# Kernel tuning notes

Measured on AMD Instinct MI355X. Metric: run time of the kernel, lower is better.

Reference implementation:

```python
import jax, jax.numpy as jnp
import numpy as np

N = 8192          # num nodes
F_IN = 512        # num_features
H = 256           # hidden_dim
D = 64            # embedding_dim
E = 262144        # num edges (avg degree 32)


def setup_inputs() -> dict:
    key = jax.random.key(0)
    ks = jax.random.split(key, 6)
    x = jax.random.normal(ks[0], (N, F_IN), dtype=jnp.float32)
    adj_rows = jax.random.randint(ks[1], (E,), 0, N)
    adj_cols = jax.random.randint(ks[2], (E,), 0, N)
    adj_vals = jax.random.uniform(ks[3], (E,), dtype=jnp.float32)
    W1 = jax.random.normal(ks[4], (F_IN, H), dtype=jnp.float32) / np.sqrt(F_IN)
    b1 = jnp.zeros((H,), dtype=jnp.float32)
    W2 = jax.random.normal(ks[5], (H, D), dtype=jnp.float32) / np.sqrt(H)
    b2 = jnp.zeros((D,), dtype=jnp.float32)
    return {"x": x, "adj_rows": adj_rows, "adj_cols": adj_cols,
            "adj_vals": adj_vals, "W1": W1, "b1": b1, "W2": W2, "b2": b2}


def _spmm(rows, cols, vals, dense):
    # sparse [N,N] @ dense [N,F] via gather + segment-sum (COO spmm)
    gathered = vals[:, None] * dense[cols]           # [E, F]
    return jax.ops.segment_sum(gathered, rows, num_segments=N)


def reference(x, adj_rows, adj_cols, adj_vals, W1, b1, W2, b2):
    # GCN layer 1: linear -> spmm -> relu (dropout is identity in eval mode)
    h = _spmm(adj_rows, adj_cols, adj_vals, x @ W1 + b1)   # [N, H]
    h = jax.nn.relu(h)
    # GCN layer 2: linear -> spmm
    z = _spmm(adj_rows, adj_cols, adj_vals, h @ W2 + b2)   # [N, D]
    # decode: sigmoid(z z^T)
    adj_rec = jax.nn.sigmoid(z @ z.T)                       # [N, N]
    return (z, adj_rec)
```

## Files before the change

### kernel.cpp

```cpp
#include <hip/hip_runtime.h>
#include <hip/hip_bf16.h>

#define NN 8192
#define FIN 512
#define HD 256
#define DD 64
#define NE 262144
#define BCAP 128

typedef __bf16 bf16_t;
typedef __bf16 bf16x8 __attribute__((ext_vector_type(8)));
typedef __bf16 bf16x4 __attribute__((ext_vector_type(4)));
typedef float f32x4 __attribute__((ext_vector_type(4)));

__global__ __launch_bounds__(256) void prep_kernel(const float* __restrict__ x, bf16_t* __restrict__ x_b,
                                                   const float* __restrict__ W1, bf16_t* __restrict__ w1t,
                                                   const float* __restrict__ W2, bf16_t* __restrict__ w2t,
                                                   int* __restrict__ deg) {
    int b = blockIdx.x;
    if (b < 2048) {
        int i = (b * 256 + threadIdx.x) * 8;
        float4 v0 = *reinterpret_cast<const float4*>(x + i);
        float4 v1 = *reinterpret_cast<const float4*>(x + i + 4);
        bf16x8 o = {(bf16_t)v0.x, (bf16_t)v0.y, (bf16_t)v0.z, (bf16_t)v0.w,
                    (bf16_t)v1.x, (bf16_t)v1.y, (bf16_t)v1.z, (bf16_t)v1.w};
        *reinterpret_cast<bf16x8*>(x_b + i) = o;
    } else if (b < 2048 + 128) {
        int o4 = ((b - 2048) * 256 + threadIdx.x) * 4;
        int r = o4 & 511;
        int c = o4 >> 9;
        bf16x4 o = {(bf16_t)W1[(r + 0) * HD + c], (bf16_t)W1[(r + 1) * HD + c],
                    (bf16_t)W1[(r + 2) * HD + c], (bf16_t)W1[(r + 3) * HD + c]};
        *reinterpret_cast<bf16x4*>(w1t + o4) = o;
    } else if (b < 2048 + 128 + 16) {
        int o4 = ((b - 2048 - 128) * 256 + threadIdx.x) * 4;
        int r = o4 & 255;
        int c = o4 >> 8;
        bf16x4 o = {(bf16_t)W2[(r + 0) * DD + c], (bf16_t)W2[(r + 1) * DD + c],
                    (bf16_t)W2[(r + 2) * DD + c], (bf16_t)W2[(r + 3) * DD + c]};
        *reinterpret_cast<bf16x4*>(w2t + o4) = o;
    } else {
        int o = ((b - 2048 - 128 - 16) * 256 + threadIdx.x) * 4;
        *reinterpret_cast<int4*>(deg + o) = {0, 0, 0, 0};
    }
}

__global__ __launch_bounds__(256) void gemm1_scatter(const bf16_t* __restrict__ A,
                                                     const bf16_t* __restrict__ Bt,
                                                     const float* __restrict__ bias,
                                                     bf16_t* __restrict__ C,
                                                     const int* __restrict__ rows, const int* __restrict__ cols,
                                                     const float* __restrict__ vals,
                                                     int* __restrict__ deg, int* __restrict__ scol,
                                                     float* __restrict__ sval) {
    int b = blockIdx.x;
    if (b >= 512) {
        int e = (b - 512) * 256 + threadIdx.x;
        int r = rows[e];
        int p = atomicAdd(&deg[r], 1);
        scol[r * BCAP + p] = cols[e];
        sval[r * BCAP + p] = vals[e];
        return;
    }
    const int K = FIN, N = HD;
    int wave = threadIdx.x >> 6;
    int lane = threadIdx.x & 63;
    int lr = lane & 15;
    int lq = lane >> 4;
    int m0 = (b & 127) * 64 + wave * 16;
    int n0 = (b >> 7) * 64;

    f32x4 acc[4];
#pragma unroll
    for (int t = 0; t < 4; t++) acc[t] = {0.f, 0.f, 0.f, 0.f};

    const bf16_t* Abase = A + (size_t)(m0 + lr) * K + lq * 8;
    const bf16_t* Bbase = Bt + (size_t)(n0 + lr) * K + lq * 8;
    for (int k0 = 0; k0 < K; k0 += 32) {
        bf16x8 a = *reinterpret_cast<const bf16x8*>(Abase + k0);
#pragma unroll
        for (int t = 0; t < 4; t++) {
            bf16x8 bb = *reinterpret_cast<const bf16x8*>(Bbase + (size_t)t * 16 * K + k0);
            acc[t] = __builtin_amdgcn_mfma_f32_16x16x32_bf16(a, bb, acc[t], 0, 0, 0);
        }
    }
#pragma unroll
    for (int t = 0; t < 4; t++) {
        int col = n0 + t * 16 + lr;
        float bv = bias[col];
#pragma unroll
        for (int r = 0; r < 4; r++) {
            int row = m0 + lq * 4 + r;
            C[(size_t)row * N + col] = (bf16_t)(acc[t][r] + bv);
        }
    }
}


__global__ __launch_bounds__(256) void spmm_h_kernel(const int* __restrict__ deg,
                                                     const int* __restrict__ scol,
                                                     const float* __restrict__ sval,
                                                     const bf16_t* __restrict__ h0,
                                                     bf16_t* __restrict__ h) {
    int r = blockIdx.x;
    int wv = threadIdx.x >> 6;
    int lane = threadIdx.x & 63;
    int nd = deg[r];
    int base = r * BCAP;
    float a0 = 0.f, a1 = 0.f, a2 = 0.f, a3 = 0.f;
#pragma unroll 2
    for (int e = wv; e < nd; e += 4) {
        int c = scol[base + e];
        float v = sval[base + e];
        bf16x4 hv = *reinterpret_cast<const bf16x4*>(h0 + (size_t)c * HD + lane * 4);
        a0 += v * (float)hv[0];
        a1 += v * (float)hv[1];
        a2 += v * (float)hv[2];
        a3 += v * (float)hv[3];
    }
    __shared__ float red[4][256];
    red[wv][lane * 4 + 0] = a0;
    red[wv][lane * 4 + 1] = a1;
    red[wv][lane * 4 + 2] = a2;
    red[wv][lane * 4 + 3] = a3;
    __syncthreads();
    if (wv == 0) {
        int f = lane * 4;
        bf16x4 o = {(bf16_t)fmaxf(red[0][f + 0] + red[1][f + 0] + red[2][f + 0] + red[3][f + 0], 0.f),
                    (bf16_t)fmaxf(red[0][f + 1] + red[1][f + 1] + red[2][f + 1] + red[3][f + 1], 0.f),
                    (bf16_t)fmaxf(red[0][f + 2] + red[1][f + 2] + red[2][f + 2] + red[3][f + 2], 0.f),
                    (bf16_t)fmaxf(red[0][f + 3] + red[1][f + 3] + red[2][f + 3] + red[3][f + 3], 0.f)};
        *reinterpret_cast<bf16x4*>(h + (size_t)r * HD + f) = o;
    }
}

__global__ __launch_bounds__(256) void spmm_z_kernel(const int* __restrict__ deg,
                                                     const int* __restrict__ scol,
                                                     const float* __restrict__ sval,
                                                     const bf16_t* __restrict__ z0,
                                                     float* __restrict__ z_out,
                                                     bf16_t* __restrict__ z_b) {
    int wv = threadIdx.x >> 6;
    int lane = threadIdx.x & 63;
    int lq = lane >> 4;
    int lr = lane & 15;
    int r = blockIdx.x * 16 + wv * 4 + lq;
    int nd = deg[r];
    int base = r * BCAP;
    float a0 = 0.f, a1 = 0.f, a2 = 0.f, a3 = 0.f;
    for (int e = 0; e < nd; e++) {
        int c = scol[base + e];
        float v = sval[base + e];
        bf16x4 zv = *reinterpret_cast<const bf16x4*>(z0 + (size_t)c * DD + lr * 4);
        a0 += v * (float)zv[0];
        a1 += v * (float)zv[1];
        a2 += v * (float)zv[2];
        a3 += v * (float)zv[3];
    }
    f32x4 of = {a0, a1, a2, a3};
    *reinterpret_cast<f32x4*>(z_out + (size_t)r * DD + lr * 4) = of;
    bf16x4 ob = {(bf16_t)a0, (bf16_t)a1, (bf16_t)a2, (bf16_t)a3};
    *reinterpret_cast<bf16x4*>(z_b + (size_t)r * DD + lr * 4) = ob;
}

template <int ACT, typename OutT, int MW>
__global__ __launch_bounds__(256) void gemm_bt(const bf16_t* __restrict__ A,
                                               const bf16_t* __restrict__ Bt,
                                               const float* __restrict__ bias,
                                               OutT* __restrict__ C,
                                               int M, int N, int K) {
    int wave = threadIdx.x >> 6;
    int lane = threadIdx.x & 63;
    int lr = lane & 15;
    int lq = lane >> 4;
    int m0 = blockIdx.x * (64 * MW) + wave * (16 * MW);
    int n0 = blockIdx.y * 64;

    f32x4 acc[MW][4];
#pragma unroll
    for (int i = 0; i < MW; i++)
#pragma unroll
        for (int t = 0; t < 4; t++) acc[i][t] = {0.f, 0.f, 0.f, 0.f};

    const bf16_t* Abase = A + (size_t)(m0 + lr) * K + lq * 8;
    const bf16_t* Bbase = Bt + (size_t)(n0 + lr) * K + lq * 8;

    for (int k0 = 0; k0 < K; k0 += 32) {
        bf16x8 a[MW];
#pragma unroll
        for (int i = 0; i < MW; i++)
            a[i] = *reinterpret_cast<const bf16x8*>(Abase + (size_t)i * 16 * K + k0);
#pragma unroll
        for (int t = 0; t < 4; t++) {
            bf16x8 b = *reinterpret_cast<const bf16x8*>(Bbase + (size_t)t * 16 * K + k0);
#pragma unroll
            for (int i = 0; i < MW; i++)
                acc[i][t] = __builtin_amdgcn_mfma_f32_16x16x32_bf16(a[i], b, acc[i][t], 0, 0, 0);
        }
    }

    if (ACT == 2) {
        __shared__ float ldsT[256 / 64 * 16 * MW][65];
        int rbase = wave * 16 * MW;
#pragma unroll
        for (int i = 0; i < MW; i++)
#pragma unroll
            for (int t = 0; t < 4; t++)
#pragma unroll
                for (int r = 0; r < 4; r++) {
                    float v = acc[i][t][r];
                    v = 1.f / (1.f + __expf(-v));
                    ldsT[rbase + i * 16 + lq * 4 + r][t * 16 + lr] = v;
                }
        int c4 = (lane & 15) * 4;
        int rr = lane >> 4;
#pragma unroll
        for (int j = 0; j < 4 * MW; j++) {
            int row_l = rbase + j * 4 + rr;
            f32x4 v = *reinterpret_cast<const f32x4*>(&ldsT[row_l][c4]);
            size_t gaddr = (size_t)(blockIdx.x * (64 * MW) + row_l) * N + n0 + c4;
            *reinterpret_cast<f32x4*>(&C[gaddr]) = v;
        }
    } else {
#pragma unroll
        for (int i = 0; i < MW; i++) {
#pragma unroll
            for (int t = 0; t < 4; t++) {
                int col = n0 + t * 16 + lr;
                float bv = bias ? bias[col] : 0.f;
#pragma unroll
                for (int r = 0; r < 4; r++) {
                    int row = m0 + i * 16 + lq * 4 + r;
                    C[(size_t)row * N + col] = (OutT)(acc[i][t][r] + bv);
                }
            }
        }
    }
}


extern "C" void kernel_launch(void* const* d_in, const int* in_sizes, int n_in,
                              void* d_out, int out_size, void* d_ws, size_t ws_size,
                              hipStream_t stream) {
    const float* x   = (const float*)d_in[0];
    const int* rows  = (const int*)d_in[1];
    const int* cols  = (const int*)d_in[2];
    const float* vals = (const float*)d_in[3];
    const float* W1  = (const float*)d_in[4];
    const float* b1  = (const float*)d_in[5];
    const float* W2  = (const float*)d_in[6];
    const float* b2  = (const float*)d_in[7];

    float* out_z   = (float*)d_out;
    float* out_adj = out_z + (size_t)NN * DD;

    char* ws = (char*)d_ws;
    size_t off = 0;
    auto alloc = [&](size_t bytes) { void* p = ws + off; off += (bytes + 255) & ~(size_t)255; return p; };
    bf16_t* x_b   = (bf16_t*)alloc((size_t)NN * FIN * 2);
    bf16_t* w1t   = (bf16_t*)alloc((size_t)HD * FIN * 2);
    bf16_t* w2t   = (bf16_t*)alloc((size_t)DD * HD * 2);
    bf16_t* h0    = (bf16_t*)alloc((size_t)NN * HD * 2);
    bf16_t* h_b   = (bf16_t*)alloc((size_t)NN * HD * 2);
    bf16_t* z0    = (bf16_t*)alloc((size_t)NN * DD * 2);
    bf16_t* z_b   = (bf16_t*)alloc((size_t)NN * DD * 2);
    int* deg      = (int*)alloc((size_t)NN * 4);
    int* scol     = (int*)alloc((size_t)NN * BCAP * 4);
    float* sval   = (float*)alloc((size_t)NN * BCAP * 4);

    prep_kernel<<<2048 + 128 + 16 + 8, 256, 0, stream>>>(x, x_b, W1, w1t, W2, w2t, deg);

    gemm1_scatter<<<512 + 1024, 256, 0, stream>>>(x_b, w1t, b1, h0,
                                                  rows, cols, vals, deg, scol, sval);

    spmm_h_kernel<<<NN, 256, 0, stream>>>(deg, scol, sval, h0, h_b);

    gemm_bt<0, bf16_t, 1><<<dim3(NN / 64, DD / 64), 256, 0, stream>>>(h_b, w2t, b2, z0, NN, DD, HD);

    spmm_z_kernel<<<NN / 16, 256, 0, stream>>>(deg, scol, sval, z0, out_z, z_b);

    gemm_bt<2, float, 2><<<dim3(NN / 128, NN / 64), 256, 0, stream>>>(z_b, z_b, nullptr, out_adj, NN, NN, DD);
}
```

Measured before the change: 387.7 us.

## Specialize z·zᵀ decoder GEMM with wide 16x256 per-wave tiles and full-row stores

```diff
diff --git a/kernel.cpp b/kernel.cpp
--- a/kernel.cpp
+++ b/kernel.cpp
@@ -163,78 +163,86 @@
     *reinterpret_cast<bf16x4*>(z_b + (size_t)r * DD + lr * 4) = ob;
 }
 
-template <int ACT, typename OutT, int MW>
-__global__ __launch_bounds__(256) void gemm_bt(const bf16_t* __restrict__ A,
-                                               const bf16_t* __restrict__ Bt,
-                                               const float* __restrict__ bias,
-                                               OutT* __restrict__ C,
-                                               int M, int N, int K) {
+__global__ __launch_bounds__(256) void gemm_bt_small(const bf16_t* __restrict__ A,
+                                                     const bf16_t* __restrict__ Bt,
+                                                     const float* __restrict__ bias,
+                                                     bf16_t* __restrict__ C,
+                                                     int M, int N, int K) {
     int wave = threadIdx.x >> 6;
     int lane = threadIdx.x & 63;
     int lr = lane & 15;
     int lq = lane >> 4;
-    int m0 = blockIdx.x * (64 * MW) + wave * (16 * MW);
+    int m0 = blockIdx.x * 64 + wave * 16;
     int n0 = blockIdx.y * 64;
 
-    f32x4 acc[MW][4];
-#pragma unroll
-    for (int i = 0; i < MW; i++)
-#pragma unroll
-        for (int t = 0; t < 4; t++) acc[i][t] = {0.f, 0.f, 0.f, 0.f};
+    f32x4 acc[4];
+#pragma unroll
+    for (int t = 0; t < 4; t++) acc[t] = {0.f, 0.f, 0.f, 0.f};
 
     const bf16_t* Abase = A + (size_t)(m0 + lr) * K + lq * 8;
     const bf16_t* Bbase = Bt + (size_t)(n0 + lr) * K + lq * 8;
-
     for (int k0 = 0; k0 < K; k0 += 32) {
-        bf16x8 a[MW];
-#pragma unroll
-        for (int i = 0; i < MW; i++)
-            a[i] = *reinterpret_cast<const bf16x8*>(Abase + (size_t)i * 16 * K + k0);
+        bf16x8 a = *reinterpret_cast<const bf16x8*>(Abase + k0);
 #pragma unroll
         for (int t = 0; t < 4; t++) {
             bf16x8 b = *reinterpret_cast<const bf16x8*>(Bbase + (size_t)t * 16 * K + k0);
-#pragma unroll
-            for (int i = 0; i < MW; i++)
-                acc[i][t] = __builtin_amdgcn_mfma_f32_16x16x32_bf16(a[i], b, acc[i][t], 0, 0, 0);
-        }
-    }
-
-    if (ACT == 2) {
-        __shared__ float ldsT[256 / 64 * 16 * MW][65];
-        int rbase = wave * 16 * MW;
-#pragma unroll
-        for (int i = 0; i < MW; i++)
-#pragma unroll
-            for (int t = 0; t < 4; t++)
-#pragma unroll
-                for (int r = 0; r < 4; r++) {
-                    float v = acc[i][t][r];
-                    v = 1.f / (1.f + __expf(-v));
-                    ldsT[rbase + i * 16 + lq * 4 + r][t * 16 + lr] = v;
-                }
-        int c4 = (lane & 15) * 4;
-        int rr = lane >> 4;
-#pragma unroll
-        for (int j = 0; j < 4 * MW; j++) {
-            int row_l = rbase + j * 4 + rr;
-            f32x4 v = *reinterpret_cast<const f32x4*>(&ldsT[row_l][c4]);
-            size_t gaddr = (size_t)(blockIdx.x * (64 * MW) + row_l) * N + n0 + c4;
-            *reinterpret_cast<f32x4*>(&C[gaddr]) = v;
-        }
-    } else {
-#pragma unroll
-        for (int i = 0; i < MW; i++) {
-#pragma unroll
-            for (int t = 0; t < 4; t++) {
-                int col = n0 + t * 16 + lr;
-                float bv = bias ? bias[col] : 0.f;
-#pragma unroll
-                for (int r = 0; r < 4; r++) {
-                    int row = m0 + i * 16 + lq * 4 + r;
-                    C[(size_t)row * N + col] = (OutT)(acc[i][t][r] + bv);
-                }
-            }
-        }
+            acc[t] = __builtin_amdgcn_mfma_f32_16x16x32_bf16(a, b, acc[t], 0, 0, 0);
+        }
+    }
+#pragma unroll
+    for (int t = 0; t < 4; t++) {
+        int col = n0 + t * 16 + lr;
+        float bv = bias[col];
+#pragma unroll
+        for (int r = 0; r < 4; r++) {
+            int row = m0 + lq * 4 + r;
+            C[(size_t)row * N + col] = (bf16_t)(acc[t][r] + bv);
+        }
+    }
+}
+
+__global__ __launch_bounds__(256) void gemm3_zzt(const bf16_t* __restrict__ Z,
+                                                 float* __restrict__ C) {
+    const int K = DD, N = NN;
+    int wave = threadIdx.x >> 6;
+    int lane = threadIdx.x & 63;
+    int lr = lane & 15;
+    int lq = lane >> 4;
+    int m0 = blockIdx.y * 64;
+    int n0 = blockIdx.x * 256;
+    int rw0 = m0 + wave * 16;
+
+    f32x4 acc[16];
+#pragma unroll
+    for (int t = 0; t < 16; t++) acc[t] = {0.f, 0.f, 0.f, 0.f};
+
+    const bf16_t* Abase = Z + (size_t)(rw0 + lr) * K + lq * 8;
+    const bf16_t* Bbase = Z + (size_t)(n0 + lr) * K + lq * 8;
+#pragma unroll
+    for (int k0 = 0; k0 < K; k0 += 32) {
+        bf16x8 a = *reinterpret_cast<const bf16x8*>(Abase + k0);
+#pragma unroll
+        for (int t = 0; t < 16; t++) {
+            bf16x8 b = *reinterpret_cast<const bf16x8*>(Bbase + (size_t)t * 16 * K + k0);
+            acc[t] = __builtin_amdgcn_mfma_f32_16x16x32_bf16(a, b, acc[t], 0, 0, 0);
+        }
+    }
+
+    __shared__ float lds[4][16 * 260];
+    float* lw = lds[wave];
+#pragma unroll
+    for (int t = 0; t < 16; t++)
+#pragma unroll
+        for (int r = 0; r < 4; r++) {
+            float v = acc[t][r];
+            v = 1.f / (1.f + __expf(-v));
+            lw[(lq * 4 + r) * 260 + t * 16 + lr] = v;
+        }
+#pragma unroll
+    for (int j = 0; j < 16; j++) {
+        f32x4 v = *reinterpret_cast<const f32x4*>(&lw[j * 260 + lane * 4]);
+        size_t gaddr = (size_t)(rw0 + j) * N + n0 + lane * 4;
+        *reinterpret_cast<f32x4*>(&C[gaddr]) = v;
     }
 }
 
@@ -275,9 +283,9 @@
 
     spmm_h_kernel<<<NN, 256, 0, stream>>>(deg, scol, sval, h0, h_b);
 
-    gemm_bt<0, bf16_t, 1><<<dim3(NN / 64, DD / 64), 256, 0, stream>>>(h_b, w2t, b2, z0, NN, DD, HD);
+    gemm_bt_small<<<dim3(NN / 64, DD / 64), 256, 0, stream>>>(h_b, w2t, b2, z0, NN, DD, HD);
 
     spmm_z_kernel<<<NN / 16, 256, 0, stream>>>(deg, scol, sval, z0, out_z, z_b);
 
-    gemm_bt<2, float, 2><<<dim3(NN / 128, NN / 64), 256, 0, stream>>>(z_b, z_b, nullptr, out_adj, NN, NN, DD);
-}
+    gemm3_zzt<<<dim3(NN / 256, NN / 64), 256, 0, stream>>>(z_b, out_adj);
+}
```

Result: slower. 420.9 us (+8.5%).

## Fuse layer-1 SpMM with ReLU and the H×W2 projection per row

Applied to the files above, without the earlier changes.

```diff
diff --git a/kernel.cpp b/kernel.cpp
--- a/kernel.cpp
+++ b/kernel.cpp
@@ -15,7 +15,7 @@
 
 __global__ __launch_bounds__(256) void prep_kernel(const float* __restrict__ x, bf16_t* __restrict__ x_b,
                                                    const float* __restrict__ W1, bf16_t* __restrict__ w1t,
-                                                   const float* __restrict__ W2, bf16_t* __restrict__ w2t,
+                                                   const float* __restrict__ W2, bf16_t* __restrict__ w2b,
                                                    int* __restrict__ deg) {
     int b = blockIdx.x;
     if (b < 2048) {
@@ -32,15 +32,15 @@
         bf16x4 o = {(bf16_t)W1[(r + 0) * HD + c], (bf16_t)W1[(r + 1) * HD + c],
                     (bf16_t)W1[(r + 2) * HD + c], (bf16_t)W1[(r + 3) * HD + c]};
         *reinterpret_cast<bf16x4*>(w1t + o4) = o;
-    } else if (b < 2048 + 128 + 16) {
-        int o4 = ((b - 2048 - 128) * 256 + threadIdx.x) * 4;
-        int r = o4 & 255;
-        int c = o4 >> 8;
-        bf16x4 o = {(bf16_t)W2[(r + 0) * DD + c], (bf16_t)W2[(r + 1) * DD + c],
-                    (bf16_t)W2[(r + 2) * DD + c], (bf16_t)W2[(r + 3) * DD + c]};
-        *reinterpret_cast<bf16x4*>(w2t + o4) = o;
+    } else if (b < 2048 + 128 + 8) {
+        int i = ((b - 2048 - 128) * 256 + threadIdx.x) * 8;
+        float4 v0 = *reinterpret_cast<const float4*>(W2 + i);
+        float4 v1 = *reinterpret_cast<const float4*>(W2 + i + 4);
+        bf16x8 o = {(bf16_t)v0.x, (bf16_t)v0.y, (bf16_t)v0.z, (bf16_t)v0.w,
+                    (bf16_t)v1.x, (bf16_t)v1.y, (bf16_t)v1.z, (bf16_t)v1.w};
+        *reinterpret_cast<bf16x8*>(w2b + i) = o;
     } else {
-        int o = ((b - 2048 - 128 - 16) * 256 + threadIdx.x) * 4;
+        int o = ((b - 2048 - 128 - 8) * 256 + threadIdx.x) * 4;
         *reinterpret_cast<int4*>(deg + o) = {0, 0, 0, 0};
     }
 }
@@ -96,41 +96,64 @@
     }
 }
 
-
-__global__ __launch_bounds__(256) void spmm_h_kernel(const int* __restrict__ deg,
-                                                     const int* __restrict__ scol,
-                                                     const float* __restrict__ sval,
-                                                     const bf16_t* __restrict__ h0,
-                                                     bf16_t* __restrict__ h) {
+__global__ __launch_bounds__(256) void spmm_h_gemm2(const int* __restrict__ deg,
+                                                    const int* __restrict__ scol,
+                                                    const float* __restrict__ sval,
+                                                    const bf16_t* __restrict__ h0,
+                                                    const bf16_t* __restrict__ w2b,
+                                                    const float* __restrict__ b2,
+                                                    bf16_t* __restrict__ z0) {
     int r = blockIdx.x;
-    int wv = threadIdx.x >> 6;
-    int lane = threadIdx.x & 63;
+    int t = threadIdx.x;
+    int wv = t >> 6;
+    int lane = t & 63;
+    int half = lane >> 5;
+    int li = lane & 31;
+    int stream = wv * 2 + half;
     int nd = deg[r];
     int base = r * BCAP;
-    float a0 = 0.f, a1 = 0.f, a2 = 0.f, a3 = 0.f;
-#pragma unroll 2
-    for (int e = wv; e < nd; e += 4) {
+
+    float a[8] = {0.f, 0.f, 0.f, 0.f, 0.f, 0.f, 0.f, 0.f};
+    for (int e = stream; e < nd; e += 8) {
         int c = scol[base + e];
         float v = sval[base + e];
-        bf16x4 hv = *reinterpret_cast<const bf16x4*>(h0 + (size_t)c * HD + lane * 4);
-        a0 += v * (float)hv[0];
-        a1 += v * (float)hv[1];
-        a2 += v * (float)hv[2];
-        a3 += v * (float)hv[3];
-    }
-    __shared__ float red[4][256];
-    red[wv][lane * 4 + 0] = a0;
-    red[wv][lane * 4 + 1] = a1;
-    red[wv][lane * 4 + 2] = a2;
-    red[wv][lane * 4 + 3] = a3;
+        const bf16_t* hp = h0 + (size_t)c * HD;
+        bf16x4 h0v = *reinterpret_cast<const bf16x4*>(hp + li * 4);
+        bf16x4 h1v = *reinterpret_cast<const bf16x4*>(hp + 128 + li * 4);
+#pragma unroll
+        for (int j = 0; j < 4; j++) a[j] += v * (float)h0v[j];
+#pragma unroll
+        for (int j = 0; j < 4; j++) a[4 + j] += v * (float)h1v[j];
+    }
+
+    __shared__ float red[8][256];
+    f32x4 w0 = {a[0], a[1], a[2], a[3]};
+    f32x4 w1 = {a[4], a[5], a[6], a[7]};
+    *reinterpret_cast<f32x4*>(&red[stream][li * 4]) = w0;
+    *reinterpret_cast<f32x4*>(&red[stream][128 + li * 4]) = w1;
     __syncthreads();
-    if (wv == 0) {
-        int f = lane * 4;
-        bf16x4 o = {(bf16_t)fmaxf(red[0][f + 0] + red[1][f + 0] + red[2][f + 0] + red[3][f + 0], 0.f),
-                    (bf16_t)fmaxf(red[0][f + 1] + red[1][f + 1] + red[2][f + 1] + red[3][f + 1], 0.f),
-                    (bf16_t)fmaxf(red[0][f + 2] + red[1][f + 2] + red[2][f + 2] + red[3][f + 2], 0.f),
-                    (bf16_t)fmaxf(red[0][f + 3] + red[1][f + 3] + red[2][f + 3] + red[3][f + 3], 0.f)};
-        *reinterpret_cast<bf16x4*>(h + (size_t)r * HD + f) = o;
+
+    __shared__ float hrow[256];
+    {
+        float s = 0.f;
+#pragma unroll
+        for (int k = 0; k < 8; k++) s += red[k][t];
+        hrow[t] = fmaxf(s, 0.f);
+    }
+    __syncthreads();
+
+    int c = t & 63, q = t >> 6;
+    float p = 0.f;
+    const bf16_t* w2p = w2b + (size_t)q * 64 * DD + c;
+#pragma unroll 8
+    for (int k = 0; k < 64; k++)
+        p += hrow[q * 64 + k] * (float)w2p[(size_t)k * DD];
+    __shared__ float part[4][64];
+    part[q][c] = p;
+    __syncthreads();
+    if (t < 64) {
+        float zv = part[0][t] + part[1][t] + part[2][t] + part[3][t] + b2[t];
+        z0[(size_t)r * DD + t] = (bf16_t)zv;
     }
 }
 
@@ -163,12 +186,10 @@
     *reinterpret_cast<bf16x4*>(z_b + (size_t)r * DD + lr * 4) = ob;
 }
 
-template <int ACT, typename OutT, int MW>
-__global__ __launch_bounds__(256) void gemm_bt(const bf16_t* __restrict__ A,
-                                               const bf16_t* __restrict__ Bt,
-                                               const float* __restrict__ bias,
-                                               OutT* __restrict__ C,
-                                               int M, int N, int K) {
+__global__ __launch_bounds__(256) void gemm3_zzt(const bf16_t* __restrict__ Z,
+                                                 float* __restrict__ C) {
+    const int K = DD, N = NN;
+    const int MW = 2;
     int wave = threadIdx.x >> 6;
     int lane = threadIdx.x & 63;
     int lr = lane & 15;
@@ -182,9 +203,9 @@
 #pragma unroll
         for (int t = 0; t < 4; t++) acc[i][t] = {0.f, 0.f, 0.f, 0.f};
 
-    const bf16_t* Abase = A + (size_t)(m0 + lr) * K + lq * 8;
-    const bf16_t* Bbase = Bt + (size_t)(n0 + lr) * K + lq * 8;
-
+    const bf16_t* Abase = Z + (size_t)(m0 + lr) * K + lq * 8;
+    const bf16_t* Bbase = Z + (size_t)(n0 + lr) * K + lq * 8;
+#pragma unroll
     for (int k0 = 0; k0 < K; k0 += 32) {
         bf16x8 a[MW];
 #pragma unroll
@@ -199,42 +220,26 @@
         }
     }
 
-    if (ACT == 2) {
-        __shared__ float ldsT[256 / 64 * 16 * MW][65];
-        int rbase = wave * 16 * MW;
-#pragma unroll
-        for (int i = 0; i < MW; i++)
-#pragma unroll
-            for (int t = 0; t < 4; t++)
-#pragma unroll
-                for (int r = 0; r < 4; r++) {
-                    float v = acc[i][t][r];
-                    v = 1.f / (1.f + __expf(-v));
-                    ldsT[rbase + i * 16 + lq * 4 + r][t * 16 + lr] = v;
-                }
-        int c4 = (lane & 15) * 4;
-        int rr = lane >> 4;
-#pragma unroll
-        for (int j = 0; j < 4 * MW; j++) {
-            int row_l = rbase + j * 4 + rr;
-            f32x4 v = *reinterpret_cast<const f32x4*>(&ldsT[row_l][c4]);
-            size_t gaddr = (size_t)(blockIdx.x * (64 * MW) + row_l) * N + n0 + c4;
-            *reinterpret_cast<f32x4*>(&C[gaddr]) = v;
-        }
-    } else {
-#pragma unroll
-        for (int i = 0; i < MW; i++) {
-#pragma unroll
-            for (int t = 0; t < 4; t++) {
-                int col = n0 + t * 16 + lr;
-                float bv = bias ? bias[col] : 0.f;
-#pragma unroll
-                for (int r = 0; r < 4; r++) {
-                    int row = m0 + i * 16 + lq * 4 + r;
-                    C[(size_t)row * N + col] = (OutT)(acc[i][t][r] + bv);
-                }
+    __shared__ float ldsT[4 * 16 * MW][65];
+    int rbase = wave * 16 * MW;
+#pragma unroll
+    for (int i = 0; i < MW; i++)
+#pragma unroll
+        for (int t = 0; t < 4; t++)
+#pragma unroll
+            for (int r = 0; r < 4; r++) {
+                float v = acc[i][t][r];
+                v = 1.f / (1.f + __expf(-v));
+                ldsT[rbase + i * 16 + lq * 4 + r][t * 16 + lr] = v;
             }
-        }
+    int c4 = (lane & 15) * 4;
+    int rr = lane >> 4;
+#pragma unroll
+    for (int j = 0; j < 4 * MW; j++) {
+        int row_l = rbase + j * 4 + rr;
+        f32x4 v = *reinterpret_cast<const f32x4*>(&ldsT[row_l][c4]);
+        size_t gaddr = (size_t)(blockIdx.x * (64 * MW) + row_l) * N + n0 + c4;
+        *reinterpret_cast<f32x4*>(&C[gaddr]) = v;
     }
 }
 
@@ -259,25 +264,22 @@
     auto alloc = [&](size_t bytes) { void* p = ws + off; off += (bytes + 255) & ~(size_t)255; return p; };
     bf16_t* x_b   = (bf16_t*)alloc((size_t)NN * FIN * 2);
     bf16_t* w1t   = (bf16_t*)alloc((size_t)HD * FIN * 2);
-    bf16_t* w2t   = (bf16_t*)alloc((size_t)DD * HD * 2);
+    bf16_t* w2b   = (bf16_t*)alloc((size_t)HD * DD * 2);
     bf16_t* h0    = (bf16_t*)alloc((size_t)NN * HD * 2);
-    bf16_t* h_b   = (bf16_t*)alloc((size_t)NN * HD * 2);
     bf16_t* z0    = (bf16_t*)alloc((size_t)NN * DD * 2);
     bf16_t* z_b   = (bf16_t*)alloc((size_t)NN * DD * 2);
     int* deg      = (int*)alloc((size_t)NN * 4);
     int* scol     = (int*)alloc((size_t)NN * BCAP * 4);
     float* sval   = (float*)alloc((size_t)NN * BCAP * 4);
 
-    prep_kernel<<<2048 + 128 + 16 + 8, 256, 0, stream>>>(x, x_b, W1, w1t, W2, w2t, deg);
+    prep_kernel<<<2048 + 128 + 8 + 8, 256, 0, stream>>>(x, x_b, W1, w1t, W2, w2b, deg);
 
     gemm1_scatter<<<512 + 1024, 256, 0, stream>>>(x_b, w1t, b1, h0,
                                                   rows, cols, vals, deg, scol, sval);
 
-    spmm_h_kernel<<<NN, 256, 0, stream>>>(deg, scol, sval, h0, h_b);
-
-    gemm_bt<0, bf16_t, 1><<<dim3(NN / 64, DD / 64), 256, 0, stream>>>(h_b, w2t, b2, z0, NN, DD, HD);
+    spmm_h_gemm2<<<NN, 256, 0, stream>>>(deg, scol, sval, h0, w2b, b2, z0);
 
     spmm_z_kernel<<<NN / 16, 256, 0, stream>>>(deg, scol, sval, z0, out_z, z_b);
 
-    gemm_bt<2, float, 2><<<dim3(NN / 128, NN / 64), 256, 0, stream>>>(z_b, z_b, nullptr, out_adj, NN, NN, DD);
-}
+    gemm3_zzt<<<dim3(NN / 128, NN / 64), 256, 0, stream>>>(z_b, out_adj);
+}
```

Result: no change. 394.7 us (+1.8%).
